# Kernel optimization log

Measured on AMD Instinct MI355X. Metric: run time of the kernel, lower is better.

Reference implementation:

```python
import jax, jax.numpy as jnp
import numpy as np

N = 4096   # num nodes
D = 512    # hidden_dim
H = 8      # head_num (hardcoded in module)
E = 131072 # num relation pairs
DH = D // H


def setup_inputs() -> dict:
    key = jax.random.key(0)
    k1, k2, k3, k4, k5, k6 = jax.random.split(key, 6)
    inst_feature = jax.random.normal(k1, (N, D), jnp.float32)
    aggregator_matrix = jax.random.randint(k2, (N, N), 0, 2).astype(jnp.float32)
    # unique (sub, obj) pairs to avoid nondeterministic duplicate scatter-set
    rng = np.random.default_rng(0)
    flat = rng.choice(N * N, size=E, replace=False)
    rel_pair_index = jnp.stack(
        [jnp.asarray(flat // N, jnp.int32), jnp.asarray(flat % N, jnp.int32)], axis=1)
    std = np.sqrt(2.0 / (D + DH)).astype(np.float32)
    w_q = jax.random.normal(k3, (D, D), jnp.float32) * std
    w_k = jax.random.normal(k4, (D, D), jnp.float32) * std
    bnd = 1.0 / np.sqrt(D)
    b_q = jax.random.uniform(k5, (D,), jnp.float32, -bnd, bnd)
    b_k = jax.random.uniform(k6, (D,), jnp.float32, -bnd, bnd)
    return {"inst_feature": inst_feature, "aggregator_matrix": aggregator_matrix,
            "rel_pair_index": rel_pair_index, "w_q": w_q, "b_q": b_q,
            "w_k": w_k, "b_k": b_k}


def reference(inst_feature, aggregator_matrix, rel_pair_index, w_q, b_q, w_k, b_k):
    n, d = inst_feature.shape
    sub = rel_pair_index[:, 0]
    obj = rel_pair_index[:, 1]
    # gather + project (eval mode: dropouts are identity)
    q = (inst_feature[sub] @ w_q.T + b_q).reshape(-1, H, DH)  # [E,H,dh]
    k = (inst_feature[obj] @ w_k.T + b_k).reshape(-1, H, DH)  # [E,H,dh]
    scores = (q * k).sum(-1) / np.sqrt(DH).astype(np.float32)  # [E,H]
    # scatter into dense [H,N,N]
    af = jnp.zeros((H, n, n), inst_feature.dtype).at[:, sub, obj].set(scores.T)
    # mask where aggregator_matrix == 0 (applied before diagonal override)
    af = jnp.where((aggregator_matrix == 0)[None], -jnp.inf, af)
    diag = jnp.arange(n)
    af = af.at[:, diag, diag].set(1e-7)
    p = jax.nn.softmax(af, axis=2)          # softmax over last dim
    factor = p.sum(axis=0) / H              # [N,N]
    return factor @ inst_feature            # [N,D]
```

## Files before the change

### kernel.cpp

```cpp
#include <hip/hip_runtime.h>

#define N_INST 4096
#define D_FEAT 512
#define NHEAD 8
#define NPAIR 131072

typedef __attribute__((ext_vector_type(8))) short short8;
typedef __attribute__((ext_vector_type(4))) float f32x4;
typedef __attribute__((ext_vector_type(4))) unsigned short u16x4;

__device__ inline unsigned short f2bf(float f) {
  union { float f; unsigned u; } v; v.f = f;
  unsigned r = v.u + 0x7fffu + ((v.u >> 16) & 1u);
  return (unsigned short)(r >> 16);
}
__device__ inline float bf2f(unsigned short b) {
  union { unsigned u; float f; } v; v.u = ((unsigned)b) << 16; return v.f;
}
__device__ inline void gload16(const void* g, void* l) {
  __builtin_amdgcn_global_load_lds((const __attribute__((address_space(1))) unsigned int*)g,
                                   (__attribute__((address_space(3))) unsigned int*)l, 16, 0, 0);
}

__global__ __launch_bounds__(256) void k_castw(const float* __restrict__ wq,
                                               const float* __restrict__ wk,
                                               unsigned short* __restrict__ dst) {
  const float* src = blockIdx.y ? wk : wq;
  unsigned short* d = dst + (size_t)blockIdx.y * D_FEAT * D_FEAT;
  int i = (blockIdx.x * 256 + threadIdx.x) * 4;
  float4 v = *(const float4*)&src[i];
  ushort4 o;
  o.x = f2bf(v.x); o.y = f2bf(v.y); o.z = f2bf(v.z); o.w = f2bf(v.w);
  *(ushort4*)&d[i] = o;
}

__global__ __launch_bounds__(256) void k_xprep(const float* __restrict__ x,
                                               unsigned short* __restrict__ xb,
                                               unsigned short* __restrict__ xT) {
  __shared__ float t[32][33];
  int bx = blockIdx.x, by = blockIdx.y;
  int tx = threadIdx.x & 31, ty = threadIdx.x >> 5;
  #pragma unroll
  for (int r = 0; r < 4; ++r) {
    int row = by * 32 + ty + r * 8;
    float v = x[(size_t)row * D_FEAT + bx * 32 + tx];
    t[ty + r * 8][tx] = v;
    xb[(size_t)row * D_FEAT + bx * 32 + tx] = f2bf(v);
  }
  __syncthreads();
  #pragma unroll
  for (int r = 0; r < 4; ++r)
    xT[(size_t)(bx * 32 + ty + r * 8) * N_INST + by * 32 + tx] = f2bf(t[tx][ty + r * 8]);
}

__global__ __launch_bounds__(256) void k_mask_acnt(const float* __restrict__ agg,
                                                   unsigned short* __restrict__ maskb,
                                                   int* __restrict__ acnt) {
  int i = blockIdx.x;
  const f32x4* row = (const f32x4*)(agg + (size_t)i * N_INST);
  u16x4* mrow = (u16x4*)(maskb + (size_t)i * N_INST);
  int tid = threadIdx.x;
  f32x4 v[4];
  #pragma unroll
  for (int u = 0; u < 4; ++u)
    v[u] = __builtin_nontemporal_load(&row[u * 256 + tid]);
  int cnt = 0;
  #pragma unroll
  for (int u = 0; u < 4; ++u) {
    int t = u * 256 + tid;
    u16x4 m;
    m[0] = (v[u][0] != 0.f) ? 0x3F80 : 0;
    m[1] = (v[u][1] != 0.f) ? 0x3F80 : 0;
    m[2] = (v[u][2] != 0.f) ? 0x3F80 : 0;
    m[3] = (v[u][3] != 0.f) ? 0x3F80 : 0;
    cnt += (v[u][0] != 0.f) + (v[u][1] != 0.f) + (v[u][2] != 0.f) + (v[u][3] != 0.f);
    int j = t * 4;
    if (i >= j && i < j + 4) {
      int d = i - j;
      m[d] = 0x3F80;
      cnt -= (v[u][d] != 0.f);
    }
    __builtin_nontemporal_store(m, &mrow[t]);
  }
  #pragma unroll
  for (int msk = 1; msk < 64; msk <<= 1) cnt += __shfl_xor(cnt, msk);
  __shared__ int wsum[4];
  if ((threadIdx.x & 63) == 0) wsum[threadIdx.x >> 6] = cnt;
  __syncthreads();
  if (threadIdx.x == 0) acnt[i] = wsum[0] + wsum[1] + wsum[2] + wsum[3];
}

template<int BIAS, int CBF16, int BN>
__global__ __launch_bounds__(256, 2) void k_gemm(const unsigned short* __restrict__ A,
                                                 const unsigned short* __restrict__ B,
                                                 const float* __restrict__ bias0,
                                                 const float* __restrict__ bias1,
                                                 void* __restrict__ Cv,
                                                 int M, int N, int K, int klen) {
  constexpr int NI = BN / 32;
  constexpr int BCH = BN / 32;
  __shared__ __align__(16) unsigned short lA[2][128 * 64];
  __shared__ __align__(16) unsigned short lB[2][BN * 64];
  int tid = threadIdx.x, wave = tid >> 6, lane = tid & 63;
  int wm = wave & 1, wn = wave >> 1;
  int gx = gridDim.x;
  int nxy = gx * gridDim.y;
  int lin = blockIdx.x + gx * blockIdx.y;
  int nch = nxy >> 3;
  int nl = (lin & 7) * nch + (lin >> 3);
  int bx = nl % gx, by = nl / gx;
  int bm = by * 128, bn = bx * BN;
  int kbase = blockIdx.z * klen;
  int srow = lane >> 3;
  int sg = (lane & 7) ^ srow;
  const unsigned short* ag[4];
  const unsigned short* bg[BCH];
  #pragma unroll
  for (int p = 0; p < 4; ++p) {
    int row = (wave * 4 + p) * 8 + srow;
    ag[p] = A + (size_t)(bm + row) * K + kbase + sg * 8;
  }
  #pragma unroll
  for (int p = 0; p < BCH; ++p) {
    int row = (wave * BCH + p) * 8 + srow;
    bg[p] = B + (size_t)(bn + row) * K + kbase + sg * 8;
  }
  auto stage = [&](int buf) {
    #pragma unroll
    for (int p = 0; p < 4; ++p) { gload16(ag[p], &lA[buf][(wave * 4 + p) * 512]); ag[p] += 64; }
    #pragma unroll
    for (int p = 0; p < BCH; ++p) { gload16(bg[p], &lB[buf][(wave * BCH + p) * 512]); bg[p] += 64; }
  };
  f32x4 acc[4][NI] = {};
  int nt = klen / 64;
  stage(0);
  __syncthreads();
  int cur = 0;
  int lrow = lane & 15, glq = lane >> 4;
  for (int t = 0; t < nt; ++t) {
    if (t + 1 < nt) stage(cur ^ 1);
    short8 bf[2][NI];
    #pragma unroll
    for (int kk = 0; kk < 2; ++kk)
      #pragma unroll
      for (int ni = 0; ni < NI; ++ni) {
        int row = wn * (BN / 2) + ni * 16 + lrow;
        int pg = (kk * 4 + glq) ^ (row & 7);
        bf[kk][ni] = *(const short8*)&lB[cur][row * 64 + pg * 8];
      }
    #pragma unroll
    for (int mi = 0; mi < 4; ++mi)
      #pragma unroll
      for (int kk = 0; kk < 2; ++kk) {
        int row = wm * 64 + mi * 16 + lrow;
        int pg = (kk * 4 + glq) ^ (row & 7);
        short8 af = *(const short8*)&lA[cur][row * 64 + pg * 8];
        #pragma unroll
        for (int ni = 0; ni < NI; ++ni)
          acc[mi][ni] = __builtin_amdgcn_mfma_f32_16x16x32_bf16(af, bf[kk][ni], acc[mi][ni], 0, 0, 0);
      }
    __syncthreads();
    cur ^= 1;
  }
  #pragma unroll
  for (int mi = 0; mi < 4; ++mi)
    #pragma unroll
    for (int ni = 0; ni < NI; ++ni) {
      int col = bn + wn * (BN / 2) + ni * 16 + lrow;
      float bv = 0.f;
      if (BIAS) bv = (col < 512) ? bias0[col] : bias1[col - 512];
      #pragma unroll
      for (int j = 0; j < 4; ++j) {
        int row = bm + wm * 64 + mi * 16 + glq * 4 + j;
        float vv = acc[mi][ni][j] + bv;
        if (CBF16) {
          ((unsigned short*)Cv)[(size_t)row * N + col] = f2bf(vv);
        } else {
          float* C = (float*)Cv + (size_t)blockIdx.z * M * N;
          C[(size_t)row * N + col] = vv;
        }
      }
    }
}

__global__ __launch_bounds__(256) void k_scores(const unsigned short* __restrict__ QKb,
                                                const int* __restrict__ pairs,
                                                const float* __restrict__ agg,
                                                float* __restrict__ es,
                                                float* __restrict__ sumexp,
                                                int* __restrict__ scnt) {
  int wave = threadIdx.x >> 6, lane = threadIdx.x & 63;
  int e = blockIdx.x * 4 + wave;
  int2 pr = *(const int2*)&pairs[2 * e];
  int sub = pr.x, obj = pr.y;
  bool valid = (sub != obj) && (agg[(size_t)sub * N_INST + obj] != 0.f);
  if (!valid) {
    if (lane == 0) es[(size_t)e * 8] = -1.f;
    return;
  }
  short8 q8 = *(const short8*)&QKb[(size_t)sub * 1024 + lane * 8];
  short8 k8 = *(const short8*)&QKb[(size_t)obj * 1024 + 512 + lane * 8];
  float p = 0.f;
  #pragma unroll
  for (int j = 0; j < 8; ++j)
    p += bf2f((unsigned short)q8[j]) * bf2f((unsigned short)k8[j]);
  p += __shfl_xor(p, 1);
  p += __shfl_xor(p, 2);
  p += __shfl_xor(p, 4);
  float ev = expf(p * 0.125f);
  int h = lane >> 3;
  if ((lane & 7) == 0) {
    es[(size_t)e * 8 + h] = ev;
    atomicAdd(&sumexp[sub * 8 + h], ev);
  }
  if (lane == 0) atomicAdd(&scnt[sub], 1);
}

__global__ __launch_bounds__(256) void k_denom(const float* __restrict__ sumexp,
                                               const int* __restrict__ scnt,
                                               const int* __restrict__ acnt,
                                               float* __restrict__ invden,
                                               float* __restrict__ base) {
  int i = blockIdx.x * 256 + threadIdx.x;
  if (i >= N_INST) return;
  float c0 = (float)(acnt[i] - scnt[i]);
  const float E0 = expf(1e-7f);
  float bsum = 0.f;
  #pragma unroll
  for (int h = 0; h < NHEAD; ++h) {
    float inv = 1.0f / (E0 + c0 + sumexp[i * NHEAD + h]);
    invden[i * NHEAD + h] = inv;
    bsum += inv;
  }
  base[i] = bsum * (1.0f / NHEAD);
}

__global__ __launch_bounds__(256) void k_scatter(const int* __restrict__ pairs,
                                                 const float* __restrict__ es,
                                                 const float* __restrict__ invden,
                                                 const float* __restrict__ base,
                                                 unsigned short* __restrict__ maskb) {
  int e = blockIdx.x * 256 + threadIdx.x;
  if (e >= NPAIR) return;
  float4 e0 = *(const float4*)&es[(size_t)e * 8];
  if (e0.x < 0.f) return;
  float4 e1 = *(const float4*)&es[(size_t)e * 8 + 4];
  int sub = pairs[2 * e], obj = pairs[2 * e + 1];
  const float* inv = &invden[sub * 8];
  float f = e0.x * inv[0] + e0.y * inv[1] + e0.z * inv[2] + e0.w * inv[3] +
            e1.x * inv[4] + e1.y * inv[5] + e1.z * inv[6] + e1.w * inv[7];
  maskb[(size_t)sub * N_INST + obj] = f2bf(f * 0.125f / base[sub]);
}

__global__ __launch_bounds__(256) void k_redscale(const float* __restrict__ P,
                                                  const float* __restrict__ base,
                                                  float* __restrict__ out) {
  size_t idx = ((size_t)blockIdx.x * 256 + threadIdx.x) * 4;
  int i = (int)(idx >> 9);
  const size_t S = (size_t)N_INST * 512;
  float4 a = *(const float4*)&P[idx];
  float4 b = *(const float4*)&P[idx + S];
  float4 c = *(const float4*)&P[idx + 2 * S];
  float4 d = *(const float4*)&P[idx + 3 * S];
  float s = base[i];
  float4 o;
  o.x = s * (a.x + b.x + c.x + d.x);
  o.y = s * (a.y + b.y + c.y + d.y);
  o.z = s * (a.z + b.z + c.z + d.z);
  o.w = s * (a.w + b.w + c.w + d.w);
  *(float4*)&out[idx] = o;
}

extern "C" void kernel_launch(void* const* d_in, const int* in_sizes, int n_in,
                              void* d_out, int out_size, void* d_ws, size_t ws_size,
                              hipStream_t stream) {
  const float* x   = (const float*)d_in[0];
  const float* agg = (const float*)d_in[1];
  const int*   prs = (const int*)d_in[2];
  const float* w_q = (const float*)d_in[3];
  const float* b_q = (const float*)d_in[4];
  const float* w_k = (const float*)d_in[5];
  const float* b_k = (const float*)d_in[6];
  float* out = (float*)d_out;

  char* ws = (char*)d_ws;
  size_t off = 0;
  auto alloc = [&](size_t bytes) -> void* {
    void* p = ws + off;
    off += (bytes + 255) & ~(size_t)255;
    return p;
  };
  unsigned short* xb    = (unsigned short*)alloc((size_t)N_INST * D_FEAT * 2);
  unsigned short* xbT   = (unsigned short*)alloc((size_t)D_FEAT * N_INST * 2);
  unsigned short* wqkb  = (unsigned short*)alloc((size_t)1024 * D_FEAT * 2);
  void*           QKP   = alloc((size_t)N_INST * 512 * 4 * 4);
  float*          es    = (float*)alloc((size_t)NPAIR * NHEAD * 4);
  float*          sumexp= (float*)alloc((size_t)N_INST * NHEAD * 4);
  int*            scnt  = (int*)alloc((size_t)N_INST * 4);
  int*            acnt  = (int*)alloc((size_t)N_INST * 4);
  float*          invden= (float*)alloc((size_t)N_INST * NHEAD * 4);
  float*          base  = (float*)alloc((size_t)N_INST * 4);
  unsigned short* maskb = (unsigned short*)alloc((size_t)N_INST * N_INST * 2);

  hipMemsetAsync(sumexp, 0, (size_t)N_INST * NHEAD * 4, stream);
  hipMemsetAsync(scnt, 0, (size_t)N_INST * 4, stream);

  k_castw<<<dim3(D_FEAT * D_FEAT / 4 / 256, 2), 256, 0, stream>>>(w_q, w_k, wqkb);
  k_xprep<<<dim3(D_FEAT / 32, N_INST / 32), 256, 0, stream>>>(x, xb, xbT);
  k_mask_acnt<<<dim3(N_INST), 256, 0, stream>>>(agg, maskb, acnt);

  k_gemm<1, 1, 64><<<dim3(1024 / 64, N_INST / 128, 1), 256, 0, stream>>>(
      xb, wqkb, b_q, b_k, QKP, N_INST, 1024, D_FEAT, D_FEAT);

  k_scores<<<dim3(NPAIR / 4), 256, 0, stream>>>((const unsigned short*)QKP, prs, agg, es, sumexp, scnt);
  k_denom<<<dim3(N_INST / 256), 256, 0, stream>>>(sumexp, scnt, acnt, invden, base);
  k_scatter<<<dim3(NPAIR / 256), 256, 0, stream>>>(prs, es, invden, base, maskb);

  k_gemm<0, 0, 128><<<dim3(512 / 128, N_INST / 128, 4), 256, 0, stream>>>(
      maskb, xbT, nullptr, nullptr, QKP, N_INST, 512, N_INST, N_INST / 4);

  k_redscale<<<dim3(N_INST * 512 / 4 / 256), 256, 0, stream>>>((const float*)QKP, base, out);
}
```

Measured before the change: 120.8 us.

## Sort pairs by subject for score locality and store split-K partials in bf16

Adds a counting sort of relation pairs by subject node (histogram, single-block prefix scan, atomic permute). k_scores then reads pairs through the permutation, with a block-index remap that gives each XCD a contiguous chunk, so Q rows and the agg row are reused in cache. Separately, the split-K aggregation GEMM now writes its partials as bf16 instead of fp32, halving that write and the read in k_redscale. The costs are three extra small launches plus a memset, and lower precision in the partial sums before the reduction.

Measured after the change: 172.8 us. 1.43x slower.

```diff
diff --git a/kernel.cpp b/kernel.cpp
--- a/kernel.cpp
+++ b/kernel.cpp
@@ -174,7 +174,8 @@
         int row = bm + wm * 64 + mi * 16 + glq * 4 + j;
         float vv = acc[mi][ni][j] + bv;
         if (CBF16) {
-          ((unsigned short*)Cv)[(size_t)row * N + col] = f2bf(vv);
+          unsigned short* C = (unsigned short*)Cv + (size_t)blockIdx.z * M * N;
+          C[(size_t)row * N + col] = f2bf(vv);
         } else {
           float* C = (float*)Cv + (size_t)blockIdx.z * M * N;
           C[(size_t)row * N + col] = vv;
@@ -183,14 +184,56 @@
     }
 }
 
+__global__ __launch_bounds__(256) void k_hist(const int* __restrict__ pairs,
+                                              int* __restrict__ hist) {
+  int e = blockIdx.x * 256 + threadIdx.x;
+  if (e < NPAIR) atomicAdd(&hist[pairs[2 * e]], 1);
+}
+
+__global__ __launch_bounds__(1024) void k_prefix(const int* __restrict__ hist,
+                                                 int* __restrict__ offs) {
+  __shared__ int s[1024];
+  int t = threadIdx.x;
+  int4 h = *(const int4*)&hist[t * 4];
+  int loc = h.x + h.y + h.z + h.w;
+  s[t] = loc;
+  __syncthreads();
+  for (int d = 1; d < 1024; d <<= 1) {
+    int v = (t >= d) ? s[t - d] : 0;
+    __syncthreads();
+    s[t] += v;
+    __syncthreads();
+  }
+  int base = (t > 0) ? s[t - 1] : 0;
+  offs[t * 4]     = base;
+  offs[t * 4 + 1] = base + h.x;
+  offs[t * 4 + 2] = base + h.x + h.y;
+  offs[t * 4 + 3] = base + h.x + h.y + h.z;
+}
+
+__global__ __launch_bounds__(256) void k_permute(const int* __restrict__ pairs,
+                                                 int* __restrict__ offs,
+                                                 int* __restrict__ perm) {
+  int e = blockIdx.x * 256 + threadIdx.x;
+  if (e < NPAIR) {
+    int p = atomicAdd(&offs[pairs[2 * e]], 1);
+    perm[p] = e;
+  }
+}
+
 __global__ __launch_bounds__(256) void k_scores(const unsigned short* __restrict__ QKb,
                                                 const int* __restrict__ pairs,
+                                                const int* __restrict__ perm,
                                                 const float* __restrict__ agg,
                                                 float* __restrict__ es,
                                                 float* __restrict__ sumexp,
                                                 int* __restrict__ scnt) {
   int wave = threadIdx.x >> 6, lane = threadIdx.x & 63;
-  int e = blockIdx.x * 4 + wave;
+  int nb = gridDim.x;
+  int lin = blockIdx.x;
+  int nch = nb >> 3;
+  int nl = (lin & 7) * nch + (lin >> 3);
+  int e = perm[nl * 4 + wave];
   int2 pr = *(const int2*)&pairs[2 * e];
   int sub = pr.x, obj = pr.y;
   bool valid = (sub != obj) && (agg[(size_t)sub * N_INST + obj] != 0.f);
@@ -252,22 +295,22 @@
   maskb[(size_t)sub * N_INST + obj] = f2bf(f * 0.125f / base[sub]);
 }
 
-__global__ __launch_bounds__(256) void k_redscale(const float* __restrict__ P,
+__global__ __launch_bounds__(256) void k_redscale(const unsigned short* __restrict__ P,
                                                   const float* __restrict__ base,
                                                   float* __restrict__ out) {
   size_t idx = ((size_t)blockIdx.x * 256 + threadIdx.x) * 4;
   int i = (int)(idx >> 9);
   const size_t S = (size_t)N_INST * 512;
-  float4 a = *(const float4*)&P[idx];
-  float4 b = *(const float4*)&P[idx + S];
-  float4 c = *(const float4*)&P[idx + 2 * S];
-  float4 d = *(const float4*)&P[idx + 3 * S];
+  u16x4 a = *(const u16x4*)&P[idx];
+  u16x4 b = *(const u16x4*)&P[idx + S];
+  u16x4 c = *(const u16x4*)&P[idx + 2 * S];
+  u16x4 d = *(const u16x4*)&P[idx + 3 * S];
   float s = base[i];
   float4 o;
-  o.x = s * (a.x + b.x + c.x + d.x);
-  o.y = s * (a.y + b.y + c.y + d.y);
-  o.z = s * (a.z + b.z + c.z + d.z);
-  o.w = s * (a.w + b.w + c.w + d.w);
+  o.x = s * (bf2f(a[0]) + bf2f(b[0]) + bf2f(c[0]) + bf2f(d[0]));
+  o.y = s * (bf2f(a[1]) + bf2f(b[1]) + bf2f(c[1]) + bf2f(d[1]));
+  o.z = s * (bf2f(a[2]) + bf2f(b[2]) + bf2f(c[2]) + bf2f(d[2]));
+  o.w = s * (bf2f(a[3]) + bf2f(b[3]) + bf2f(c[3]) + bf2f(d[3]));
   *(float4*)&out[idx] = o;
 }
 
@@ -293,31 +336,39 @@
   unsigned short* xb    = (unsigned short*)alloc((size_t)N_INST * D_FEAT * 2);
   unsigned short* xbT   = (unsigned short*)alloc((size_t)D_FEAT * N_INST * 2);
   unsigned short* wqkb  = (unsigned short*)alloc((size_t)1024 * D_FEAT * 2);
-  void*           QKP   = alloc((size_t)N_INST * 512 * 4 * 4);
+  void*           QKP   = alloc((size_t)N_INST * 1024 * 2 > (size_t)N_INST * 512 * 2 * 4
+                                ? (size_t)N_INST * 1024 * 2 * 2 : (size_t)N_INST * 512 * 2 * 4);
   float*          es    = (float*)alloc((size_t)NPAIR * NHEAD * 4);
   float*          sumexp= (float*)alloc((size_t)N_INST * NHEAD * 4);
   int*            scnt  = (int*)alloc((size_t)N_INST * 4);
   int*            acnt  = (int*)alloc((size_t)N_INST * 4);
   float*          invden= (float*)alloc((size_t)N_INST * NHEAD * 4);
   float*          base  = (float*)alloc((size_t)N_INST * 4);
+  int*            hist  = (int*)alloc((size_t)N_INST * 4);
+  int*            offs  = (int*)alloc((size_t)N_INST * 4);
+  int*            perm  = (int*)alloc((size_t)NPAIR * 4);
   unsigned short* maskb = (unsigned short*)alloc((size_t)N_INST * N_INST * 2);
 
   hipMemsetAsync(sumexp, 0, (size_t)N_INST * NHEAD * 4, stream);
   hipMemsetAsync(scnt, 0, (size_t)N_INST * 4, stream);
+  hipMemsetAsync(hist, 0, (size_t)N_INST * 4, stream);
 
   k_castw<<<dim3(D_FEAT * D_FEAT / 4 / 256, 2), 256, 0, stream>>>(w_q, w_k, wqkb);
   k_xprep<<<dim3(D_FEAT / 32, N_INST / 32), 256, 0, stream>>>(x, xb, xbT);
+  k_hist<<<dim3(NPAIR / 256), 256, 0, stream>>>(prs, hist);
+  k_prefix<<<dim3(1), 1024, 0, stream>>>(hist, offs);
+  k_permute<<<dim3(NPAIR / 256), 256, 0, stream>>>(prs, offs, perm);
   k_mask_acnt<<<dim3(N_INST), 256, 0, stream>>>(agg, maskb, acnt);
 
   k_gemm<1, 1, 64><<<dim3(1024 / 64, N_INST / 128, 1), 256, 0, stream>>>(
       xb, wqkb, b_q, b_k, QKP, N_INST, 1024, D_FEAT, D_FEAT);
 
-  k_scores<<<dim3(NPAIR / 4), 256, 0, stream>>>((const unsigned short*)QKP, prs, agg, es, sumexp, scnt);
+  k_scores<<<dim3(NPAIR / 4), 256, 0, stream>>>((const unsigned short*)QKP, prs, perm, agg, es, sumexp, scnt);
   k_denom<<<dim3(N_INST / 256), 256, 0, stream>>>(sumexp, scnt, acnt, invden, base);
   k_scatter<<<dim3(NPAIR / 256), 256, 0, stream>>>(prs, es, invden, base, maskb);
 
-  k_gemm<0, 0, 128><<<dim3(512 / 128, N_INST / 128, 4), 256, 0, stream>>>(
+  k_gemm<0, 1, 128><<<dim3(512 / 128, N_INST / 128, 4), 256, 0, stream>>>(
       maskb, xbT, nullptr, nullptr, QKP, N_INST, 512, N_INST, N_INST / 4);
 
-  k_redscale<<<dim3(N_INST * 512 / 4 / 256), 256, 0, stream>>>((const float*)QKP, base, out);
-}
+  k_redscale<<<dim3(N_INST * 512 / 4 / 256), 256, 0, stream>>>((const unsigned short*)QKP, base, out);
+}
```
